# Performance work log

Hardware: AMD Instinct MI355X
Metric: run time of the kernel (lower is better)

## Reference

```python
import jax, jax.numpy as jnp
import numpy as np


def setup_inputs() -> dict:
    key = jax.random.key(0)
    ks = jax.random.split(key, 6)
    b, l, d, n, r = 2, 2048, 512, 64, 32
    x = jax.random.normal(ks[0], (b, l, d), dtype=jnp.float32)
    # x_proj: Linear(d, r + 2n, bias=False) -> weight (r+2n, d)
    W_xproj = jax.random.normal(ks[1], (r + 2 * n, d), dtype=jnp.float32) / np.sqrt(d)
    # dt_proj: Linear(r, d, bias=True)
    W_dt = jax.random.normal(ks[2], (d, r), dtype=jnp.float32) / np.sqrt(r)
    b_dt = jax.random.normal(ks[3], (d,), dtype=jnp.float32) * 0.01
    # A_log = log(repeat(arange(1, n+1), 'n -> d n'))
    A_log = jnp.log(jnp.broadcast_to(jnp.arange(1, n + 1, dtype=jnp.float32), (d, n)))
    D = jnp.ones((d,), dtype=jnp.float32)
    return {"x": x, "W_xproj": W_xproj, "W_dt": W_dt, "b_dt": b_dt, "A_log": A_log, "D": D}


def _s6_forward(x, W_xproj, W_dt, b_dt, A_log, D):
    d, n = A_log.shape
    r = W_dt.shape[1]
    A = -jnp.exp(A_log)                               # (d, n)
    x_dbl = jnp.einsum('bld,ed->ble', x, W_xproj)     # (b, l, r+2n)
    delta_r = x_dbl[..., :r]
    B = x_dbl[..., r:r + n]                           # (b, l, n)
    C = x_dbl[..., r + n:]                            # (b, l, n)
    delta = jax.nn.softplus(jnp.einsum('blr,dr->bld', delta_r, W_dt) + b_dt)  # (b, l, d)
    # discretize
    deltaA = jnp.exp(jnp.einsum('bld,dn->bldn', delta, A))        # (b, l, d, n)
    deltaB_u = jnp.einsum('bld,bln,bld->bldn', delta, B, x)       # (b, l, d, n)
    bsz = x.shape[0]
    h0 = jnp.zeros((bsz, d, n), dtype=x.dtype)

    def step(h, inp):
        dA_t, dBu_t, C_t = inp                        # (b,d,n), (b,d,n), (b,n)
        h = dA_t * h + dBu_t
        y_t = jnp.einsum('bdn,bn->bd', h, C_t)
        return h, y_t

    xs = (jnp.moveaxis(deltaA, 1, 0), jnp.moveaxis(deltaB_u, 1, 0), jnp.moveaxis(C, 1, 0))
    _, ys = jax.lax.scan(step, h0, xs)                # ys: (l, b, d)
    y = jnp.moveaxis(ys, 0, 1)                        # (b, l, d)
    return y + x * D


def reference(x, W_xproj, W_dt, b_dt, A_log, D):
    return _s6_forward(x, W_xproj, W_dt, b_dt, A_log, D)
```

## Files before the change

### kernel.cpp

```cpp
#include <hip/hip_runtime.h>
#include <cstdint>

#define Bsz 2
#define Lsz 2048
#define Dm  512
#define Nst 64
#define Rr  32
#define Ee  160
#define NCHUNK 32
#define CLEN   64
#define L2E 1.44269504f
#define LN2 0.69314718f

typedef __bf16  bf16x8 __attribute__((ext_vector_type(8)));
typedef float   f32x4  __attribute__((ext_vector_type(4)));
typedef unsigned short u16x8 __attribute__((ext_vector_type(8)));

__device__ __forceinline__ float rdlane(float v, int l) {
    return __int_as_float(__builtin_amdgcn_readlane(__float_as_int(v), l));
}
__device__ __forceinline__ float fexp2(float x) { return __builtin_amdgcn_exp2f(x); }
__device__ __forceinline__ float flog2(float x) { return __builtin_amdgcn_logf(x); }

__global__ __launch_bounds__(256) void kcast2(const float* __restrict__ a,
                                              unsigned short* __restrict__ oa, int na8,
                                              const float* __restrict__ b,
                                              unsigned short* __restrict__ ob, int nb8) {
    int gid = blockIdx.x * 256 + threadIdx.x;
    const float* in; unsigned short* op; int idx;
    if (gid < na8) { in = a; op = oa; idx = gid; }
    else { idx = gid - na8; if (idx >= nb8) return; in = b; op = ob; }
    const float4* ip = reinterpret_cast<const float4*>(in) + (size_t)idx * 2;
    float4 v0 = ip[0], v1 = ip[1];
    float vv[8] = {v0.x, v0.y, v0.z, v0.w, v1.x, v1.y, v1.z, v1.w};
    u16x8 r;
    #pragma unroll
    for (int j = 0; j < 8; ++j) {
        uint32_t u = __float_as_uint(vv[j]);
        u += 0x7FFFu + ((u >> 16) & 1u);
        r[j] = (unsigned short)(u >> 16);
    }
    *reinterpret_cast<u16x8*>(op + (size_t)idx * 8) = r;
}

__global__ __launch_bounds__(256) void k1_mfma(const unsigned short* __restrict__ xbf,
                                               const unsigned short* __restrict__ wbf,
                                               float* __restrict__ xdbl) {
    const int tid = threadIdx.x;
    const int wv = tid >> 6, lane = tid & 63;
    const int ng = blockIdx.x % 10, mg = blockIdx.x / 10;
    const int m0 = mg * 64 + wv * 16;
    const int n0 = ng * 16;
    const int ra = lane & 15, kg = lane >> 4;
    const unsigned short* ap = xbf + (size_t)(m0 + ra) * Dm + kg * 8;
    const unsigned short* bp = wbf + (size_t)(n0 + ra) * Dm + kg * 8;
    f32x4 acc = {0.f, 0.f, 0.f, 0.f};
    #pragma unroll
    for (int ks = 0; ks < 16; ++ks) {
        bf16x8 a = *reinterpret_cast<const bf16x8*>(ap + ks * 32);
        bf16x8 b = *reinterpret_cast<const bf16x8*>(bp + ks * 32);
        acc = __builtin_amdgcn_mfma_f32_16x16x32_bf16(a, b, acc, 0, 0, 0);
    }
    float* dp = xdbl + (size_t)(m0 + kg * 4) * Ee + n0 + ra;
    dp[0]      = acc[0];
    dp[Ee]     = acc[1];
    dp[2 * Ee] = acc[2];
    dp[3 * Ee] = acc[3];
}

__global__ __launch_bounds__(256) void k2_delta(const float* __restrict__ xdbl,
                                                const float* __restrict__ x,
                                                const float* __restrict__ Wdt,
                                                const float* __restrict__ bdt,
                                                float* __restrict__ delta_t,
                                                float* __restrict__ du_t,
                                                float* __restrict__ sumdl) {
    __shared__ float dr[64][33];
    __shared__ float wd[64][32];
    __shared__ float pt[64][65];
    const int tid = threadIdx.x;
    const int lt = blockIdx.x & 31;
    const int dt = (blockIdx.x >> 5) & 7;
    const int b  = blockIdx.x >> 8;
    const int l0 = lt * 64, d0 = dt * 64;

    for (int i = tid; i < 512; i += 256) {
        int l = i >> 3, j4 = i & 7;
        const float4 v = *reinterpret_cast<const float4*>(
            xdbl + (size_t)(b * Lsz + l0 + l) * Ee + j4 * 4);
        dr[l][j4 * 4 + 0] = v.x; dr[l][j4 * 4 + 1] = v.y;
        dr[l][j4 * 4 + 2] = v.z; dr[l][j4 * 4 + 3] = v.w;
    }
    for (int i = tid; i < 512; i += 256) {
        int dd = i >> 3, j4 = i & 7;
        *reinterpret_cast<float4*>(&wd[dd][j4 * 4]) =
            *reinterpret_cast<const float4*>(Wdt + (size_t)(d0 + dd) * Rr + j4 * 4);
    }
    __syncthreads();

    const int w = tid >> 6, lane = tid & 63;
    float drr[32];
    #pragma unroll
    for (int j = 0; j < 32; ++j) drr[j] = dr[lane][j];

    float xv[16];
    {
        const float* xp = x + (size_t)(b * Lsz + l0 + lane) * Dm + d0 + w * 16;
        #pragma unroll
        for (int q = 0; q < 4; ++q) {
            float4 v = reinterpret_cast<const float4*>(xp)[q];
            xv[q*4] = v.x; xv[q*4+1] = v.y; xv[q*4+2] = v.z; xv[q*4+3] = v.w;
        }
    }

    float dl[16];
    #pragma unroll
    for (int i = 0; i < 16; ++i) {
        int dd = w * 16 + i;
        float z = bdt[d0 + dd];
        const float4* wr = reinterpret_cast<const float4*>(&wd[dd][0]);
        #pragma unroll
        for (int j4 = 0; j4 < 8; ++j4) {
            float4 wv = wr[j4];
            z = fmaf(drr[j4*4+0], wv.x, z);
            z = fmaf(drr[j4*4+1], wv.y, z);
            z = fmaf(drr[j4*4+2], wv.z, z);
            z = fmaf(drr[j4*4+3], wv.w, z);
        }
        float t = fexp2(-fabsf(z) * L2E);
        dl[i] = fmaxf(z, 0.f) + flog2(1.f + t) * LN2;
    }

    #pragma unroll
    for (int i = 0; i < 16; ++i) pt[w * 16 + i][lane] = dl[i];
    __syncthreads();
    for (int i = tid; i < 4096; i += 256) {
        int dd = i >> 6, ll = i & 63;
        delta_t[((size_t)(b * Dm + d0 + dd)) * Lsz + l0 + ll] = pt[dd][ll];
    }
    if (tid < 64) {
        float s = 0.f;
        #pragma unroll 16
        for (int q = 0; q < 64; ++q) s += pt[tid][q];
        sumdl[(size_t)(b * Dm + d0 + tid) * NCHUNK + lt] = s;
    }
    __syncthreads();
    #pragma unroll
    for (int i = 0; i < 16; ++i) pt[w * 16 + i][lane] = dl[i] * xv[i];
    __syncthreads();
    for (int i = tid; i < 4096; i += 256) {
        int dd = i >> 6, ll = i & 63;
        du_t[((size_t)(b * Dm + d0 + dd)) * Lsz + l0 + ll] = pt[dd][ll];
    }
}

__global__ __launch_bounds__(256) void k3a(const float* __restrict__ delta_t,
                                           const float* __restrict__ du_t,
                                           const float* __restrict__ xdbl,
                                           const float* __restrict__ Alog,
                                           float* __restrict__ hf) {
    __shared__ float Bs[64][64];
    const int tid = threadIdx.x;
    const int w = __builtin_amdgcn_readfirstlane(tid >> 6);
    const int lane = tid & 63;
    const int c   = blockIdx.x & 31;
    const int grp = blockIdx.x >> 5;
    const int chan0 = grp * 16 + w * 4;
    const int b = chan0 >> 9;
    const int t0 = c * CLEN;
    const float* __restrict__ xb0 = xdbl + ((size_t)b * Lsz + t0) * Ee;
    for (int i = tid; i < 1024; i += 256) {
        int row = i >> 4, q = i & 15;
        float4 v = *reinterpret_cast<const float4*>(xb0 + row * Ee + Rr + q * 4);
        *reinterpret_cast<float4*>(&Bs[row][q * 4]) = v;
    }
    float A2[4], h[4], dreg[4], ureg[4];
    #pragma unroll
    for (int ch = 0; ch < 4; ++ch) {
        const int cc = chan0 + ch;
        A2[ch] = -expf(Alog[(size_t)(cc & 511) * Nst + lane]) * L2E;
        dreg[ch] = delta_t[(size_t)cc * Lsz + t0 + lane];
        ureg[ch] = du_t   [(size_t)cc * Lsz + t0 + lane];
        h[ch] = 0.f;
    }
    __syncthreads();
    #pragma unroll 8
    for (int j = 0; j < CLEN; ++j) {
        float Bv = Bs[j][lane];
        #pragma unroll
        for (int ch = 0; ch < 4; ++ch) {
            float sd = rdlane(dreg[ch], j);
            float su = rdlane(ureg[ch], j);
            h[ch] = fmaf(fexp2(sd * A2[ch]), h[ch], su * Bv);
        }
    }
    #pragma unroll
    for (int ch = 0; ch < 4; ++ch)
        hf[((size_t)(chan0 + ch) * NCHUNK + c) * Nst + lane] = h[ch];
}

__global__ __launch_bounds__(256) void k3b(const float* __restrict__ Alog,
                                           const float* __restrict__ sumdl,
                                           float* __restrict__ hf) {
    const int tid = threadIdx.x;
    const int w = tid >> 6, lane = tid & 63;
    const int chan = blockIdx.x * 4 + w;
    const int d = chan & 511;
    const float A2 = -expf(Alog[(size_t)d * Nst + lane]) * L2E;
    const float sv = sumdl[chan * NCHUNK + (lane & 31)];
    const size_t base = (size_t)chan * NCHUNK * Nst + lane;
    float hv[8], nx[8];
    #pragma unroll
    for (int i = 0; i < 8; ++i) hv[i] = hf[base + i * Nst];
    float h0 = 0.f;
    for (int g = 0; g < 4; ++g) {
        if (g < 3) {
            #pragma unroll
            for (int i = 0; i < 8; ++i) nx[i] = hf[base + ((g + 1) * 8 + i) * Nst];
        }
        #pragma unroll
        for (int i = 0; i < 8; ++i) {
            const int c = g * 8 + i;
            float P = fexp2(A2 * rdlane(sv, c));
            hf[base + c * Nst] = h0;
            h0 = fmaf(P, h0, hv[i]);
        }
        #pragma unroll
        for (int i = 0; i < 8; ++i) hv[i] = nx[i];
    }
}

__global__ __launch_bounds__(256, 4) void k3c(const float* __restrict__ delta_t,
                                              const float* __restrict__ du_t,
                                              const float* __restrict__ xdbl,
                                              const float* __restrict__ Alog,
                                              const float* __restrict__ h0s,
                                              const float* __restrict__ x,
                                              const float* __restrict__ Dv,
                                              float* __restrict__ out) {
    __shared__ float BC[32][128];
    __shared__ float part[4][8][65];
    __shared__ float ystage[4][8][66];
    const int tid = threadIdx.x;
    const int w = __builtin_amdgcn_readfirstlane(tid >> 6);
    const int lane = tid & 63;
    const int c   = blockIdx.x & 31;
    const int grp = blockIdx.x >> 5;
    const int chan0 = grp * 32 + w * 8;
    const int b = chan0 >> 9;
    const int t0 = c * CLEN;
    const float* __restrict__ xb0 = xdbl + ((size_t)b * Lsz + t0) * Ee;

    float A2[8], h[8], dreg[8], ureg[8];
    #pragma unroll
    for (int ch = 0; ch < 8; ++ch) {
        const int cc = chan0 + ch;
        A2[ch] = -expf(Alog[(size_t)(cc & 511) * Nst + lane]) * L2E;
        dreg[ch] = delta_t[(size_t)cc * Lsz + t0 + lane];
        ureg[ch] = du_t   [(size_t)cc * Lsz + t0 + lane];
        h[ch] = h0s[((size_t)cc * NCHUNK + c) * Nst + lane];
    }
    const int r8 = lane & 7, sg = lane >> 3;

    #pragma unroll
    for (int half = 0; half < 2; ++half) {
        if (half) __syncthreads();
        for (int i = tid; i < 1024; i += 256) {
            int row = i >> 5, q4 = i & 31;
            float4 v = *reinterpret_cast<const float4*>(
                xb0 + (half * 32 + row) * Ee + Rr + q4 * 4);
            *reinterpret_cast<float4*>(&BC[row][q4 * 4]) = v;
        }
        __syncthreads();
        #pragma unroll 8
        for (int tt = 0; tt < 32; ++tt) {
            const int t = half * 32 + tt;
            float Bv = BC[tt][lane];
            float Cv = BC[tt][64 + lane];
            #pragma unroll
            for (int ch = 0; ch < 8; ++ch) {
                float sd = rdlane(dreg[ch], t);
                float su = rdlane(ureg[ch], t);
                h[ch] = fmaf(fexp2(sd * A2[ch]), h[ch], su * Bv);
                part[w][ch][lane] = h[ch] * Cv;
            }
            float v = 0.f;
            #pragma unroll
            for (int q = 0; q < 8; ++q) v += part[w][r8][sg * 8 + q];
            v += __shfl_xor(v, 8);
            v += __shfl_xor(v, 16);
            v += __shfl_xor(v, 32);
            if (lane < 8) ystage[w][lane][t] = v;
        }
    }
    __syncthreads();
    const int d0 = (grp * 32) & 511;
    for (int i = tid; i < 2048; i += 256) {
        int t = i >> 5, dd = i & 31;
        size_t gi = ((size_t)(b * Lsz + t0 + t)) * Dm + d0 + dd;
        out[gi] = ystage[dd >> 3][dd & 7][t] + x[gi] * Dv[d0 + dd];
    }
}

extern "C" void kernel_launch(void* const* d_in, const int* in_sizes, int n_in,
                              void* d_out, int out_size, void* d_ws, size_t ws_size,
                              hipStream_t stream) {
    const float* x    = (const float*)d_in[0];
    const float* Wxp  = (const float*)d_in[1];
    const float* Wdt  = (const float*)d_in[2];
    const float* bdt  = (const float*)d_in[3];
    const float* Alog = (const float*)d_in[4];
    const float* Dv   = (const float*)d_in[5];
    float* out = (float*)d_out;

    float* ws = (float*)d_ws;
    float*          xdbl    = ws;
    unsigned short* xbf     = (unsigned short*)(ws + 655360);
    unsigned short* wbf     = (unsigned short*)(ws + 1703936);
    float*          delta_t = ws + 1744896;
    float*          du_t    = ws + 3842048;
    float*          hf      = ws + 5939200;
    float*          sumdl   = ws + 8036352;

    hipLaunchKernelGGL(kcast2,  dim3(1064), dim3(256), 0, stream, x, xbf, 262144, Wxp, wbf, 10240);
    hipLaunchKernelGGL(k1_mfma, dim3(640),  dim3(256), 0, stream, xbf, wbf, xdbl);
    hipLaunchKernelGGL(k2_delta,dim3(512),  dim3(256), 0, stream, xdbl, x, Wdt, bdt, delta_t, du_t, sumdl);
    hipLaunchKernelGGL(k3a,     dim3(2048), dim3(256), 0, stream, delta_t, du_t, xdbl, Alog, hf);
    hipLaunchKernelGGL(k3b,     dim3(256),  dim3(256), 0, stream, Alog, sumdl, hf);
    hipLaunchKernelGGL(k3c,     dim3(1024), dim3(256), 0, stream, delta_t, du_t, xdbl, Alog, hf, x, Dv, out);
}
```

Baseline: 121.0 us.

## Software-pipeline B/C staging and defer per-step reduction in scan kernel

The chunk-scan kernel now stages B/C rows in four 16-row slices, prefetching the next slice into registers while computing the current one. The per-step dot-product reduction is delayed by one timestep and reads the partial sums with vectorized float4 LDS loads, so it overlaps with the next step's recurrence. The part array is padded to 68 columns to keep float4 reads aligned. Smaller LDS use and a launch-bounds hint of 6 blocks per CU aim to raise occupancy, at the cost of more barriers and tighter register limits.

Result: faster. 117.0 us (-3.3%).

```diff
diff --git a/kernel.cpp b/kernel.cpp
--- a/kernel.cpp
+++ b/kernel.cpp
@@ -230,7 +230,7 @@
     }
 }
 
-__global__ __launch_bounds__(256, 4) void k3c(const float* __restrict__ delta_t,
+__global__ __launch_bounds__(256, 6) void k3c(const float* __restrict__ delta_t,
                                               const float* __restrict__ du_t,
                                               const float* __restrict__ xdbl,
                                               const float* __restrict__ Alog,
@@ -238,8 +238,8 @@
                                               const float* __restrict__ x,
                                               const float* __restrict__ Dv,
                                               float* __restrict__ out) {
-    __shared__ float BC[32][128];
-    __shared__ float part[4][8][65];
+    __shared__ float BC[16][128];
+    __shared__ float part[4][8][68];
     __shared__ float ystage[4][8][66];
     const int tid = threadIdx.x;
     const int w = __builtin_amdgcn_readfirstlane(tid >> 6);
@@ -249,7 +249,7 @@
     const int chan0 = grp * 32 + w * 8;
     const int b = chan0 >> 9;
     const int t0 = c * CLEN;
-    const float* __restrict__ xb0 = xdbl + ((size_t)b * Lsz + t0) * Ee;
+    const float* __restrict__ xb0 = xdbl + ((size_t)b * Lsz + t0) * Ee + Rr;
 
     float A2[8], h[8], dreg[8], ureg[8];
     #pragma unroll
@@ -261,20 +261,29 @@
         h[ch] = h0s[((size_t)cc * NCHUNK + c) * Nst + lane];
     }
     const int r8 = lane & 7, sg = lane >> 3;
-
-    #pragma unroll
-    for (int half = 0; half < 2; ++half) {
-        if (half) __syncthreads();
-        for (int i = tid; i < 1024; i += 256) {
-            int row = i >> 5, q4 = i & 31;
-            float4 v = *reinterpret_cast<const float4*>(
-                xb0 + (half * 32 + row) * Ee + Rr + q4 * 4);
-            *reinterpret_cast<float4*>(&BC[row][q4 * 4]) = v;
-        }
+    const int srow = tid >> 5, scol = (tid & 31) * 4;
+
+    float4 pf0 = *reinterpret_cast<const float4*>(xb0 + srow * Ee + scol);
+    float4 pf1 = *reinterpret_cast<const float4*>(xb0 + (srow + 8) * Ee + scol);
+
+    for (int q = 0; q < 4; ++q) {
         __syncthreads();
-        #pragma unroll 8
-        for (int tt = 0; tt < 32; ++tt) {
-            const int t = half * 32 + tt;
+        *reinterpret_cast<float4*>(&BC[srow][scol]) = pf0;
+        *reinterpret_cast<float4*>(&BC[srow + 8][scol]) = pf1;
+        if (q < 3) {
+            pf0 = *reinterpret_cast<const float4*>(xb0 + ((q + 1) * 16 + srow) * Ee + scol);
+            pf1 = *reinterpret_cast<const float4*>(xb0 + ((q + 1) * 16 + srow + 8) * Ee + scol);
+        }
+        __syncthreads();
+        #pragma unroll
+        for (int tt = 0; tt < 16; ++tt) {
+            const int t = q * 16 + tt;
+            float4 pa, pb;
+            const bool doRed = (tt > 0) || (q > 0);
+            if (doRed) {
+                pa = *reinterpret_cast<const float4*>(&part[w][r8][sg * 8]);
+                pb = *reinterpret_cast<const float4*>(&part[w][r8][sg * 8 + 4]);
+            }
             float Bv = BC[tt][lane];
             float Cv = BC[tt][64 + lane];
             #pragma unroll
@@ -284,14 +293,21 @@
                 h[ch] = fmaf(fexp2(sd * A2[ch]), h[ch], su * Bv);
                 part[w][ch][lane] = h[ch] * Cv;
             }
-            float v = 0.f;
-            #pragma unroll
-            for (int q = 0; q < 8; ++q) v += part[w][r8][sg * 8 + q];
-            v += __shfl_xor(v, 8);
-            v += __shfl_xor(v, 16);
-            v += __shfl_xor(v, 32);
-            if (lane < 8) ystage[w][lane][t] = v;
-        }
+            if (doRed) {
+                float v = ((pa.x + pa.y) + (pa.z + pa.w)) + ((pb.x + pb.y) + (pb.z + pb.w));
+                v += __shfl_xor(v, 8);
+                v += __shfl_xor(v, 16);
+                v += __shfl_xor(v, 32);
+                if (lane < 8) ystage[w][lane][t - 1] = v;
+            }
+        }
+    }
+    {
+        float4 pa = *reinterpret_cast<const float4*>(&part[w][r8][sg * 8]);
+        float4 pb = *reinterpret_cast<const float4*>(&part[w][r8][sg * 8 + 4]);
+        float v = ((pa.x + pa.y) + (pa.z + pa.w)) + ((pb.x + pb.y) + (pb.z + pb.w));
+        v += __shfl_xor(v, 8); v += __shfl_xor(v, 16); v += __shfl_xor(v, 32);
+        if (lane < 8) ystage[w][lane][63] = v;
     }
     __syncthreads();
     const int d0 = (grp * 32) & 511;
```
